# Performance work log

Measured on AMD Instinct MI355X. Metric: run time of the kernel, lower is better.

Reference implementation:

```python
import jax, jax.numpy as jnp
import numpy as np

DIM = 32
N_TOKENS = 4
HIDDEN = 2 * DIM
BATCH = 262144
EPS = 1e-5
SCALE = 1.0 / float(np.sqrt(DIM))


def _ln(x, g, b):
    m = jnp.mean(x, axis=-1, keepdims=True)
    v = jnp.mean((x - m) ** 2, axis=-1, keepdims=True)
    return (x - m) * jax.lax.rsqrt(v + EPS) * g + b


def setup_inputs() -> dict:
    key = jax.random.key(0)
    ks = jax.random.split(key, 16)
    s = 0.02
    lin = lambda k, i, o: jax.random.normal(k, (i, o), jnp.float32) * s
    return {
        "x": jax.random.normal(ks[0], (BATCH, N_TOKENS, DIM), jnp.float32),
        "w_pe": lin(ks[1], DIM, DIM),
        "b_pe": jnp.zeros((DIM,), jnp.float32),
        "pos": jax.random.normal(ks[2], (1, N_TOKENS, DIM), jnp.float32) * s,
        "ln1_g": jnp.ones((DIM,), jnp.float32),
        "ln1_b": jnp.zeros((DIM,), jnp.float32),
        "wq": lin(ks[3], DIM, DIM), "bq": jnp.zeros((DIM,), jnp.float32),
        "wk": lin(ks[4], DIM, DIM), "bk": jnp.zeros((DIM,), jnp.float32),
        "wv": lin(ks[5], DIM, DIM), "bv": jnp.zeros((DIM,), jnp.float32),
        "wo": lin(ks[6], DIM, DIM), "bo": jnp.zeros((DIM,), jnp.float32),
        "ln2_g": jnp.ones((DIM,), jnp.float32),
        "ln2_b": jnp.zeros((DIM,), jnp.float32),
        "w1": lin(ks[7], DIM, HIDDEN), "bf1": jnp.zeros((HIDDEN,), jnp.float32),
        "w2": lin(ks[8], HIDDEN, DIM), "bf2": jnp.zeros((DIM,), jnp.float32),
    }


def reference(x, w_pe, b_pe, pos, ln1_g, ln1_b, wq, bq, wk, bk, wv, bv,
              wo, bo, ln2_g, ln2_b, w1, bf1, w2, bf2):
    # patch embed + positional embedding
    x = x @ w_pe + b_pe + pos                      # [B, T, D]
    # attention block
    xa = _ln(x, ln1_g, ln1_b)
    q = xa @ wq + bq
    k = xa @ wk + bk
    v = xa @ wv + bv
    scores = jnp.einsum("btd,bsd->bts", q, k) * SCALE  # [B, T, T]
    attn = jax.nn.softmax(scores, axis=-1)
    mixed = jnp.einsum("bts,bsd->btd", attn, v)
    x = x + mixed @ wo + bo
    # MLP block (gelu tanh approximation, matching F.gelu(approximate='tanh'))
    xb = _ln(x, ln2_g, ln2_b)
    h = jax.nn.gelu(xb @ w1 + bf1, approximate=True)   # [B, T, 2D]
    x = x + h @ w2 + bf2
    return x
```

## Files before the change

### kernel.cpp

```cpp
#include <hip/hip_runtime.h>
#include <hip/hip_bf16.h>

typedef float          f32x4  __attribute__((ext_vector_type(4)));
typedef __bf16         bf16x8 __attribute__((ext_vector_type(8)));
typedef unsigned short u16x8  __attribute__((ext_vector_type(8)));
typedef unsigned int   u32;

#define DEV static __device__ __forceinline__

static constexpr int   NT       = 65536;
static constexpr float SCALE_Q2 = 0.2550349f;

DEV unsigned short f2bf(float f) {
  return __builtin_bit_cast(unsigned short, __float2bfloat16(f));
}
DEV u32 pk2(float lo, float hi) {
  u32 r;
  asm("v_cvt_pk_bf16_f32 %0, %1, %2" : "=v"(r) : "v"(lo), "v"(hi));
  return r;
}

DEV u16x8 pack8(f32x4 a, f32x4 b) {
  uint4 q;
  q.x = pk2(a[0], a[1]); q.y = pk2(a[2], a[3]);
  q.z = pk2(b[0], b[1]); q.w = pk2(b[2], b[3]);
  return __builtin_bit_cast(u16x8, q);
}

DEV f32x4 mfma(u16x8 a, u16x8 b, f32x4 c) {
  return __builtin_amdgcn_mfma_f32_16x16x32_bf16(
      __builtin_bit_cast(bf16x8, a), __builtin_bit_cast(bf16x8, b), c, 0, 0, 0);
}
DEV void wait_lds() {
  asm volatile("s_waitcnt lgkmcnt(0)" ::: "memory");
  __builtin_amdgcn_sched_barrier(0);
}

DEV u16x8 build_frag(const float* W, int N, int k0, int col, float scale) {
  u16x8 f;
#pragma unroll
  for (int e = 0; e < 8; ++e)
    f[e] = f2bf(W[(k0 + e) * N + col] * scale);
  return f;
}
DEV u16x8 fold_frag(u16x8 f, const float* gv) {
  u16x8 o;
#pragma unroll
  for (int e = 0; e < 8; ++e) {
    union { u32 i; float v; } u; u.i = ((u32)f[e]) << 16;
    o[e] = f2bf(u.v * gv[e]);
  }
  return o;
}

DEV u16x8 conv_std(u32* buf, int r15, int lg, f32x4 a0, f32x4 a1) {
  const int wb = r15 * 20 + 2 * lg;
  buf[wb + 0] = pk2(a0[0], a0[1]);
  buf[wb + 1] = pk2(a0[2], a0[3]);
  buf[wb + 8] = pk2(a1[0], a1[1]);
  buf[wb + 9] = pk2(a1[2], a1[3]);
  wait_lds();
  uint4 rd = *(const uint4*)(buf + r15 * 20 + 4 * lg);
  return __builtin_bit_cast(u16x8, rd);
}

DEV void conv_qk(u32* bq_, u32* bk_, int r15, int lg,
                 f32x4 q0, f32x4 q1, f32x4 k0, f32x4 k1,
                 u16x8& qf, u16x8& kf) {
  const int wb = r15 * 20 + 2 * lg;
  bq_[wb + 0] = pk2(q0[0], q0[1]);
  bq_[wb + 1] = pk2(q0[2], q0[3]);
  bq_[wb + 8] = pk2(q1[0], q1[1]);
  bq_[wb + 9] = pk2(q1[2], q1[3]);
  bk_[wb + 0] = pk2(k0[0], k0[1]);
  bk_[wb + 1] = pk2(k0[2], k0[3]);
  bk_[wb + 8] = pk2(k1[0], k1[1]);
  bk_[wb + 9] = pk2(k1[2], k1[3]);
  wait_lds();
  qf = __builtin_bit_cast(u16x8, *(const uint4*)(bq_ + r15 * 20 + 4 * lg));
  kf = __builtin_bit_cast(u16x8, *(const uint4*)(bk_ + r15 * 20 + 4 * lg));
}

DEV void ln_stats(f32x4 a, f32x4 b, float& rs, float& nm) {
  float s1 = 0.f, s2 = 0.f;
#pragma unroll
  for (int i = 0; i < 4; ++i) { s1 += a[i]; s2 = fmaf(a[i], a[i], s2); }
#pragma unroll
  for (int i = 0; i < 4; ++i) { s1 += b[i]; s2 = fmaf(b[i], b[i], s2); }
  s1 += __shfl_xor(s1, 16); s2 += __shfl_xor(s2, 16);
  s1 += __shfl_xor(s1, 32); s2 += __shfl_xor(s2, 32);
  const float m   = s1 * 0.03125f;
  const float var = fmaf(s2, 0.03125f, -m * m);
  rs = __builtin_amdgcn_rsqf(var + 1e-5f);
  nm = -m * rs;
}

DEV float gelu_t(float u) {
  const float z = u * fmaf(u * u, 0.1029428f, 2.3022083f);
  const float e = __builtin_amdgcn_exp2f(z);
  return fmaf(-u, __builtin_amdgcn_rcpf(e + 1.0f), u);
}

__global__ __launch_bounds__(256) void vit_fused(
    const float* __restrict__ x,
    const float* __restrict__ wpe, const float* __restrict__ bpe,
    const float* __restrict__ pos,
    const float* __restrict__ ln1g, const float* __restrict__ ln1b,
    const float* __restrict__ wq, const float* __restrict__ bq,
    const float* __restrict__ wk, const float* __restrict__ bk,
    const float* __restrict__ wv, const float* __restrict__ bv,
    const float* __restrict__ wo, const float* __restrict__ bo,
    const float* __restrict__ ln2g, const float* __restrict__ ln2b,
    const float* __restrict__ w1, const float* __restrict__ bf1,
    const float* __restrict__ w2, const float* __restrict__ bf2,
    float* __restrict__ out) {
  const int tid = (int)threadIdx.x;
  const int wid = tid >> 6;
  const int l   = tid & 63;
  const int r15 = l & 15;
  const int lg  = l >> 4;
  const int tk  = l & 3;

  __shared__ alignas(16) u32   s_conv[4][2][320];
  __shared__ alignas(16) float s_vh[4][576];
  __shared__ alignas(16) float s_at[4][64];
  u32*   bufA = s_conv[wid][0];
  u32*   bufB = s_conv[wid][1];
  float* vS   = s_vh[wid];
  u32*   hB   = (u32*)s_vh[wid];
  float* aT   = s_at[wid];

  float g1v[8], g2v[8];
#pragma unroll
  for (int e = 0; e < 8; ++e) { g1v[e] = ln1g[8 * lg + e]; g2v[e] = ln2g[8 * lg + e]; }
  const u16x8 b1f = pack8(*(const f32x4*)(ln1b + 8 * lg), *(const f32x4*)(ln1b + 8 * lg + 4));
  const u16x8 b2f = pack8(*(const f32x4*)(ln2b + 8 * lg), *(const f32x4*)(ln2b + 8 * lg + 4));

  u16x8 wpeF[2], wqF[2], wkF[2], wvF[2], woF[2], w1F[4], w2F[2][2];
  f32x4 comboC[2], bqC[2], bkC[2], bvC[2], boC[2], bf2C[2], bf1C[4];

#pragma unroll
  for (int H = 0; H < 2; ++H) {
    const int dc  = 16 * H + 4 * lg;
    const int col = 16 * H + r15;
    wpeF[H]   = build_frag(wpe, 32, 8 * lg, col, 1.f);
    woF[H]    = build_frag(wo,  32, 8 * lg, col, 1.f);
    w2F[0][H] = build_frag(w2,  32, 8 * lg,      col, 1.f);
    w2F[1][H] = build_frag(w2,  32, 32 + 8 * lg, col, 1.f);
    f32x4 cq, ck, cv, cmb, cbo, cb2;
#pragma unroll
    for (int i = 0; i < 4; ++i) {
      const int d = dc + i;
      cmb[i] = bpe[d] + pos[tk * 32 + d];
      cq[i]  = SCALE_Q2 * bq[d];
      ck[i]  = bk[d];
      cv[i]  = bv[d];
      cbo[i] = bo[d];
      cb2[i] = bf2[d];
    }
    comboC[H] = cmb; boC[H] = cbo; bf2C[H] = cb2;
    const u16x8 rq = build_frag(wq, 32, 8 * lg, col, SCALE_Q2);
    const u16x8 rk = build_frag(wk, 32, 8 * lg, col, 1.f);
    const u16x8 rv = build_frag(wv, 32, 8 * lg, col, 1.f);
    bqC[H] = mfma(rq, b1f, cq);
    bkC[H] = mfma(rk, b1f, ck);
    bvC[H] = mfma(rv, b1f, cv);
    wqF[H] = fold_frag(rq, g1v);
    wkF[H] = fold_frag(rk, g1v);
    wvF[H] = fold_frag(rv, g1v);
  }
#pragma unroll
  for (int Hp = 0; Hp < 4; ++Hp) {
    const int col = 16 * Hp + r15;
    const u16x8 r1 = build_frag(w1, 64, 8 * lg, col, 1.f);
    f32x4 c1;
#pragma unroll
    for (int i = 0; i < 4; ++i) c1[i] = bf1[16 * Hp + 4 * lg + i];
    bf1C[Hp] = mfma(r1, b2f, c1);
    w1F[Hp]  = fold_frag(r1, g2v);
  }

  const f32x4 zero4 = {0.f, 0.f, 0.f, 0.f};
  const int stride = (int)(gridDim.x << 2);
  int tile = (int)(blockIdx.x << 2) | wid;

  const float* xp = x + (size_t)(tile * 16 + r15) * 32 + 8 * lg;
  f32x4 xv0 = *(const f32x4*)(xp);
  f32x4 xv1 = *(const f32x4*)(xp + 4);
  for (; tile < NT; tile += stride) {
    const int nxt = tile + stride;
    f32x4 nx0 = xv0, nx1 = xv1;
    if (nxt < NT) {
      const float* np_ = x + (size_t)(nxt * 16 + r15) * 32 + 8 * lg;
      nx0 = *(const f32x4*)(np_);
      nx1 = *(const f32x4*)(np_ + 4);
    }
    const u16x8 xf = pack8(xv0, xv1);

    f32x4 x1a = mfma(wpeF[0], xf, comboC[0]);
    f32x4 x1b = mfma(wpeF[1], xf, comboC[1]);

    float rs, nm;
    ln_stats(x1a, x1b, rs, nm);
    f32x4 ya, yb;
#pragma unroll
    for (int i = 0; i < 4; ++i) { ya[i] = fmaf(x1a[i], rs, nm); yb[i] = fmaf(x1b[i], rs, nm); }
    const u16x8 xaf = conv_std(bufA, r15, lg, ya, yb);

    const f32x4 qa0 = mfma(wqF[0], xaf, bqC[0]);
    const f32x4 qa1 = mfma(wqF[1], xaf, bqC[1]);
    const f32x4 ka0 = mfma(wkF[0], xaf, bkC[0]);
    const f32x4 ka1 = mfma(wkF[1], xaf, bkC[1]);
    const f32x4 va0 = mfma(wvF[0], xaf, bvC[0]);
    const f32x4 va1 = mfma(wvF[1], xaf, bvC[1]);

    *(f32x4*)(vS + r15 * 36 + 4 * lg)      = va0;
    *(f32x4*)(vS + r15 * 36 + 16 + 4 * lg) = va1;

    u16x8 qf, kf;
    conv_qk(bufB, bufA, r15, lg, qa0, qa1, ka0, ka1, qf, kf);

    const f32x4 sc = mfma(kf, qf, zero4);
    {
      const float mx = fmaxf(fmaxf(sc[0], sc[1]), fmaxf(sc[2], sc[3]));
      const float e0 = __builtin_amdgcn_exp2f(sc[0] - mx);
      const float e1 = __builtin_amdgcn_exp2f(sc[1] - mx);
      const float e2 = __builtin_amdgcn_exp2f(sc[2] - mx);
      const float e3 = __builtin_amdgcn_exp2f(sc[3] - mx);
      const float rc = __builtin_amdgcn_rcpf((e0 + e1) + (e2 + e3));
      f32x4 p; p[0] = e0 * rc; p[1] = e1 * rc; p[2] = e2 * rc; p[3] = e3 * rc;
      if (lg == (r15 >> 2)) *(f32x4*)(aT + 4 * r15) = p;
    }
    wait_lds();

    const f32x4 atv = *(const f32x4*)(aT + 4 * r15);
    f32x4 m0 = zero4, m1 = zero4;
#pragma unroll
    for (int j = 0; j < 4; ++j) {
      const f32x4 v0 = *(const f32x4*)(vS + ((r15 & 12) + j) * 36 + 4 * lg);
      const f32x4 v1 = *(const f32x4*)(vS + ((r15 & 12) + j) * 36 + 16 + 4 * lg);
      m0 += atv[j] * v0;
      m1 += atv[j] * v1;
    }
    const u16x8 mf = conv_std(bufB, r15, lg, m0, m1);

    const f32x4 x2a = mfma(woF[0], mf, x1a) + boC[0];
    const f32x4 x2b = mfma(woF[1], mf, x1b) + boC[1];

    ln_stats(x2a, x2b, rs, nm);
#pragma unroll
    for (int i = 0; i < 4; ++i) { ya[i] = fmaf(x2a[i], rs, nm); yb[i] = fmaf(x2b[i], rs, nm); }
    const u16x8 xbf = conv_std(bufA, r15, lg, ya, yb);

#pragma unroll
    for (int Hp = 0; Hp < 4; ++Hp) {
      const f32x4 h = mfma(w1F[Hp], xbf, bf1C[Hp]);
      const int hb = r15 * 36 + 8 * Hp + 2 * lg;
      hB[hb]     = pk2(gelu_t(h[0]), gelu_t(h[1]));
      hB[hb + 1] = pk2(gelu_t(h[2]), gelu_t(h[3]));
    }
    wait_lds();
    const uint4 h0r = *(const uint4*)(hB + r15 * 36 + 4 * lg);
    const uint4 h1r = *(const uint4*)(hB + r15 * 36 + 16 + 4 * lg);
    const u16x8 hf0 = __builtin_bit_cast(u16x8, h0r);
    const u16x8 hf1 = __builtin_bit_cast(u16x8, h1r);

    f32x4 o0 = x2a + bf2C[0];
    f32x4 o1 = x2b + bf2C[1];
    o0 = mfma(w2F[0][0], hf0, o0);
    o0 = mfma(w2F[1][0], hf1, o0);
    o1 = mfma(w2F[0][1], hf0, o1);
    o1 = mfma(w2F[1][1], hf1, o1);

    float* op = out + (size_t)(tile * 16 + r15) * 32;
    *(f32x4*)(op + 4 * lg)      = o0;
    *(f32x4*)(op + 16 + 4 * lg) = o1;

    xv0 = nx0; xv1 = nx1;
  }
}

extern "C" void kernel_launch(void* const* d_in, const int* in_sizes, int n_in,
                              void* d_out, int out_size, void* d_ws, size_t ws_size,
                              hipStream_t stream) {
  (void)in_sizes; (void)n_in; (void)d_ws; (void)ws_size; (void)out_size;
  const float* x    = (const float*)d_in[0];
  const float* wpe  = (const float*)d_in[1];
  const float* bpe  = (const float*)d_in[2];
  const float* pos  = (const float*)d_in[3];
  const float* ln1g = (const float*)d_in[4];
  const float* ln1b = (const float*)d_in[5];
  const float* wq   = (const float*)d_in[6];
  const float* bq   = (const float*)d_in[7];
  const float* wk   = (const float*)d_in[8];
  const float* bk   = (const float*)d_in[9];
  const float* wv   = (const float*)d_in[10];
  const float* bv   = (const float*)d_in[11];
  const float* wo   = (const float*)d_in[12];
  const float* bo   = (const float*)d_in[13];
  const float* ln2g = (const float*)d_in[14];
  const float* ln2b = (const float*)d_in[15];
  const float* w1   = (const float*)d_in[16];
  const float* bf1  = (const float*)d_in[17];
  const float* w2   = (const float*)d_in[18];
  const float* bf2  = (const float*)d_in[19];

  vit_fused<<<1024, 256, 0, stream>>>(x, wpe, bpe, pos, ln1g, ln1b, wq, bq, wk, bk,
                                      wv, bv, wo, bo, ln2g, ln2b, w1, bf1, w2, bf2,
                                      (float*)d_out);
}
```

Measured before the change: 78.39 us.

## Fold output projection into V before attention mix and broadcast probs via bpermute

```diff
diff --git a/kernel.cpp b/kernel.cpp
--- a/kernel.cpp
+++ b/kernel.cpp
@@ -53,32 +53,19 @@
   return o;
 }
 
-DEV u16x8 conv_std(u32* buf, int r15, int lg, f32x4 a0, f32x4 a1) {
-  const int wb = r15 * 20 + 2 * lg;
+DEV void conv_wr(u32* buf, int wb, f32x4 a0, f32x4 a1) {
   buf[wb + 0] = pk2(a0[0], a0[1]);
   buf[wb + 1] = pk2(a0[2], a0[3]);
   buf[wb + 8] = pk2(a1[0], a1[1]);
   buf[wb + 9] = pk2(a1[2], a1[3]);
+}
+DEV u16x8 conv_rd(const u32* buf, int rb) {
+  return __builtin_bit_cast(u16x8, *(const uint4*)(buf + rb));
+}
+DEV u16x8 conv_std(u32* buf, int r15, int lg, f32x4 a0, f32x4 a1) {
+  conv_wr(buf, r15 * 20 + 2 * lg, a0, a1);
   wait_lds();
-  uint4 rd = *(const uint4*)(buf + r15 * 20 + 4 * lg);
-  return __builtin_bit_cast(u16x8, rd);
-}
-
-DEV void conv_qk(u32* bq_, u32* bk_, int r15, int lg,
-                 f32x4 q0, f32x4 q1, f32x4 k0, f32x4 k1,
-                 u16x8& qf, u16x8& kf) {
-  const int wb = r15 * 20 + 2 * lg;
-  bq_[wb + 0] = pk2(q0[0], q0[1]);
-  bq_[wb + 1] = pk2(q0[2], q0[3]);
-  bq_[wb + 8] = pk2(q1[0], q1[1]);
-  bq_[wb + 9] = pk2(q1[2], q1[3]);
-  bk_[wb + 0] = pk2(k0[0], k0[1]);
-  bk_[wb + 1] = pk2(k0[2], k0[3]);
-  bk_[wb + 8] = pk2(k1[0], k1[1]);
-  bk_[wb + 9] = pk2(k1[2], k1[3]);
-  wait_lds();
-  qf = __builtin_bit_cast(u16x8, *(const uint4*)(bq_ + r15 * 20 + 4 * lg));
-  kf = __builtin_bit_cast(u16x8, *(const uint4*)(bk_ + r15 * 20 + 4 * lg));
+  return conv_rd(buf, r15 * 20 + 4 * lg);
 }
 
 DEV void ln_stats(f32x4 a, f32x4 b, float& rs, float& nm) {
@@ -123,12 +110,11 @@
 
   __shared__ alignas(16) u32   s_conv[4][2][320];
   __shared__ alignas(16) float s_vh[4][576];
-  __shared__ alignas(16) float s_at[4][64];
   u32*   bufA = s_conv[wid][0];
   u32*   bufB = s_conv[wid][1];
   float* vS   = s_vh[wid];
+  u32*   vStg = (u32*)s_vh[wid];
   u32*   hB   = (u32*)s_vh[wid];
-  float* aT   = s_at[wid];
 
   float g1v[8], g2v[8];
 #pragma unroll
@@ -214,26 +200,38 @@
     const f32x4 va0 = mfma(wvF[0], xaf, bvC[0]);
     const f32x4 va1 = mfma(wvF[1], xaf, bvC[1]);
 
-    *(f32x4*)(vS + r15 * 36 + 4 * lg)      = va0;
-    *(f32x4*)(vS + r15 * 36 + 16 + 4 * lg) = va1;
-
-    u16x8 qf, kf;
-    conv_qk(bufB, bufA, r15, lg, qa0, qa1, ka0, ka1, qf, kf);
+    const int wb = r15 * 20 + 2 * lg;
+    conv_wr(bufB, wb, qa0, qa1);
+    conv_wr(bufA, wb, ka0, ka1);
+    conv_wr(vStg, wb, va0, va1);
+    wait_lds();
+    const int rb = r15 * 20 + 4 * lg;
+    const u16x8 qf = conv_rd(bufB, rb);
+    const u16x8 kf = conv_rd(bufA, rb);
+    const u16x8 vf = conv_rd(vStg, rb);
+
+    const f32x4 vo0 = mfma(woF[0], vf, boC[0]);
+    const f32x4 vo1 = mfma(woF[1], vf, boC[1]);
 
     const f32x4 sc = mfma(kf, qf, zero4);
-    {
-      const float mx = fmaxf(fmaxf(sc[0], sc[1]), fmaxf(sc[2], sc[3]));
-      const float e0 = __builtin_amdgcn_exp2f(sc[0] - mx);
-      const float e1 = __builtin_amdgcn_exp2f(sc[1] - mx);
-      const float e2 = __builtin_amdgcn_exp2f(sc[2] - mx);
-      const float e3 = __builtin_amdgcn_exp2f(sc[3] - mx);
-      const float rc = __builtin_amdgcn_rcpf((e0 + e1) + (e2 + e3));
-      f32x4 p; p[0] = e0 * rc; p[1] = e1 * rc; p[2] = e2 * rc; p[3] = e3 * rc;
-      if (lg == (r15 >> 2)) *(f32x4*)(aT + 4 * r15) = p;
-    }
+    const float mx = fmaxf(fmaxf(sc[0], sc[1]), fmaxf(sc[2], sc[3]));
+    const float e0 = __builtin_amdgcn_exp2f(sc[0] - mx);
+    const float e1 = __builtin_amdgcn_exp2f(sc[1] - mx);
+    const float e2 = __builtin_amdgcn_exp2f(sc[2] - mx);
+    const float e3 = __builtin_amdgcn_exp2f(sc[3] - mx);
+    const float rc = __builtin_amdgcn_rcpf((e0 + e1) + (e2 + e3));
+
+    *(f32x4*)(vS + r15 * 36 + 4 * lg)      = vo0;
+    *(f32x4*)(vS + r15 * 36 + 16 + 4 * lg) = vo1;
+
+    const int srcb = (16 * (r15 >> 2) + r15) << 2;
+    f32x4 atv;
+    atv[0] = __builtin_bit_cast(float, __builtin_amdgcn_ds_bpermute(srcb, __builtin_bit_cast(int, e0 * rc)));
+    atv[1] = __builtin_bit_cast(float, __builtin_amdgcn_ds_bpermute(srcb, __builtin_bit_cast(int, e1 * rc)));
+    atv[2] = __builtin_bit_cast(float, __builtin_amdgcn_ds_bpermute(srcb, __builtin_bit_cast(int, e2 * rc)));
+    atv[3] = __builtin_bit_cast(float, __builtin_amdgcn_ds_bpermute(srcb, __builtin_bit_cast(int, e3 * rc)));
     wait_lds();
 
-    const f32x4 atv = *(const f32x4*)(aT + 4 * r15);
     f32x4 m0 = zero4, m1 = zero4;
 #pragma unroll
     for (int j = 0; j < 4; ++j) {
@@ -242,10 +240,8 @@
       m0 += atv[j] * v0;
       m1 += atv[j] * v1;
     }
-    const u16x8 mf = conv_std(bufB, r15, lg, m0, m1);
-
-    const f32x4 x2a = mfma(woF[0], mf, x1a) + boC[0];
-    const f32x4 x2b = mfma(woF[1], mf, x1b) + boC[1];
+    const f32x4 x2a = x1a + m0;
+    const f32x4 x2b = x1b + m1;
 
     ln_stats(x2a, x2b, rs, nm);
 #pragma unroll
@@ -260,10 +256,8 @@
       hB[hb + 1] = pk2(gelu_t(h[2]), gelu_t(h[3]));
     }
     wait_lds();
-    const uint4 h0r = *(const uint4*)(hB + r15 * 36 + 4 * lg);
-    const uint4 h1r = *(const uint4*)(hB + r15 * 36 + 16 + 4 * lg);
-    const u16x8 hf0 = __builtin_bit_cast(u16x8, h0r);
-    const u16x8 hf1 = __builtin_bit_cast(u16x8, h1r);
+    const u16x8 hf0 = __builtin_bit_cast(u16x8, *(const uint4*)(hB + r15 * 36 + 4 * lg));
+    const u16x8 hf1 = __builtin_bit_cast(u16x8, *(const uint4*)(hB + r15 * 36 + 16 + 4 * lg));
 
     f32x4 o0 = x2a + bf2C[0];
     f32x4 o1 = x2b + bf2C[1];
```

Result: slower. 81.71 us (+4.2%).
